# Optimization experiments

Measured on AMD Instinct MI355X. Metric: run time of the kernel, lower is better.

Reference implementation:

```python
import jax, jax.numpy as jnp
import numpy as np

N_NODES = 1024
CHANNELS = [1, 64, 128]
DENSE = [196608, 256]
SAMPLE_NUMBER = 50


def _glorot(key, shape):
    fan_in, fan_out = shape[0], shape[-1]
    s = jnp.sqrt(6.0 / (fan_in + fan_out))
    return jax.random.uniform(key, shape, jnp.float32, -s, s)


def setup_inputs() -> dict:
    key = jax.random.key(0)
    ks = jax.random.split(key, 20)
    T, B = 16, 64
    inp = {
        "xs_seq": jax.random.normal(ks[0], (T, B, N_NODES, CHANNELS[0]), jnp.float32),
        "adj": jax.random.uniform(ks[1], (N_NODES, N_NODES), jnp.float32) / N_NODES,
    }
    # GCGRU params per layer: gates z, r, candidate n over concat([x, h])
    ki = 2
    for li in range(len(CHANNELS) - 1):
        cin, cout = CHANNELS[li], CHANNELS[li + 1]
        for g in ("z", "r", "n"):
            inp[f"W{g}{li}"] = _glorot(ks[ki], (cin + cout, cout)); ki += 1
            inp[f"b{g}{li}"] = jnp.zeros((cout,), jnp.float32)
    inp["W_mu"] = _glorot(ks[ki], (DENSE[0], DENSE[1])); ki += 1
    inp["b_mu"] = jnp.zeros((DENSE[1],), jnp.float32)
    inp["W_lv"] = _glorot(ks[ki], (DENSE[0], DENSE[1])); ki += 1
    inp["b_lv"] = jnp.zeros((DENSE[1],), jnp.float32)
    return inp


def _gcgru(xs, adj, Wz, bz, Wr, br, Wn, bn, cout):
    # xs: [T, B, N, cin]; graph-conv GRU over time via scan
    T, B, N, _ = xs.shape
    h0 = jnp.zeros((B, N, cout), xs.dtype)

    def gconv(a, x, W, b):  # adj @ x @ W + b
        return jnp.einsum("ij,bjc,cd->bid", a, x, W) + b

    def step(h, x):
        xh = jnp.concatenate([x, h], axis=-1)
        z = jax.nn.sigmoid(gconv(adj, xh, Wz, bz))
        r = jax.nn.sigmoid(gconv(adj, xh, Wr, br))
        xrh = jnp.concatenate([x, r * h], axis=-1)
        n = jnp.tanh(gconv(adj, xrh, Wn, bn))
        h_new = (1.0 - z) * h + z * n
        return h_new, h_new

    _, hs = jax.lax.scan(step, h0, xs)
    return hs  # [T, B, N, cout]


def _forward(xs_seq, adj, Wz0, bz0, Wr0, br0, Wn0, bn0,
             Wz1, bz1, Wr1, br1, Wn1, bn1, W_mu, b_mu, W_lv, b_lv, eps):
    h1 = _gcgru(xs_seq, adj, Wz0, bz0, Wr0, br0, Wn0, bn0, CHANNELS[1])
    h2 = _gcgru(h1, adj, Wz1, bz1, Wr1, br1, Wn1, bn1, CHANNELS[2])
    xs = jnp.concatenate([h1[-1], h2[-1]], axis=2)  # [B, N, C1+C2]
    B = xs.shape[0]
    xs = xs.reshape(B, -1)  # [B, N*(C1+C2)]
    mu = jax.nn.sigmoid(xs @ W_mu + b_mu)
    logvar = jax.nn.sigmoid(xs @ W_lv + b_lv)
    std = jnp.exp(0.5 * logvar)
    z = mu + eps * std
    return z, mu, logvar


def reference(xs_seq, adj, Wz0, bz0, Wr0, br0, Wn0, bn0,
              Wz1, bz1, Wr1, br1, Wn1, bn1, W_mu, b_mu, W_lv, b_lv):
    B = xs_seq.shape[1]
    ekey = jax.random.fold_in(jax.random.key(0), 1234)
    eps = jax.random.normal(ekey, (SAMPLE_NUMBER, B, DENSE[1]), jnp.float32).mean(0)
    return _forward(xs_seq, adj, Wz0, bz0, Wr0, br0, Wn0, bn0,
                    Wz1, bz1, Wr1, br1, Wn1, bn1, W_mu, b_mu, W_lv, b_lv, eps)
```

## Files before the change

kernel.cpp:

```cpp
#include <hip/hip_runtime.h>
#include <math.h>

#define EPS_MODE 0

typedef unsigned short u16;
typedef short bf16x8 __attribute__((ext_vector_type(8)));
typedef float f32x4 __attribute__((ext_vector_type(4)));
typedef u16 u16x4 __attribute__((ext_vector_type(4)));
typedef u16 u16x8 __attribute__((ext_vector_type(8)));

static constexpr int T = 16;
static constexpr size_t MF = 1u << 20;
static constexpr int DKCH = 256;
static constexpr int DKCHUNK = 196608 / DKCH;

__device__ __forceinline__ u16 f2bf(float f) {
  unsigned u = __float_as_uint(f);
  unsigned r = (u + 0x7fffu + ((u >> 16) & 1u)) >> 16;
  return (u16)r;
}
__device__ __forceinline__ float bf2f(u16 h) {
  return __uint_as_float(((unsigned)h) << 16);
}
__device__ __forceinline__ void gload16(const void* g, void* l) {
  __builtin_amdgcn_global_load_lds(
      (const __attribute__((address_space(1))) void*)g,
      (__attribute__((address_space(3))) void*)l, 16, 0, 0);
}

__global__ __launch_bounds__(256) void cast_bf16(const float* __restrict__ in,
                                                 u16* __restrict__ out, int n) {
  int i = (blockIdx.x * 256 + threadIdx.x) * 4;
  if (i < n) {
    float4 v = *reinterpret_cast<const float4*>(&in[i]);
    out[i + 0] = f2bf(v.x); out[i + 1] = f2bf(v.y);
    out[i + 2] = f2bf(v.z); out[i + 3] = f2bf(v.w);
  }
}

__global__ __launch_bounds__(256) void prep_wt(const float* __restrict__ Wz0, const float* __restrict__ Wr0,
                                               const float* __restrict__ Wn0, const float* __restrict__ Wz1,
                                               const float* __restrict__ Wr1, const float* __restrict__ Wn1,
                                               u16* __restrict__ WzrT0, u16* __restrict__ WnT0,
                                               u16* __restrict__ WzrT1, u16* __restrict__ WnT1) {
  int seg = blockIdx.y;
  int idx = blockIdx.x * 256 + threadIdx.x;
  if (seg == 0) {
    if (idx < 128 * 64) {
      int j = idx >> 6, k = idx & 63;
      float v = (j < 64) ? Wz0[(k + 1) * 64 + j] : Wr0[(k + 1) * 64 + (j - 64)];
      WzrT0[idx] = f2bf(v);
    }
  } else if (seg == 1) {
    if (idx < 64 * 64) {
      int j = idx >> 6, k = idx & 63;
      WnT0[idx] = f2bf(Wn0[(k + 1) * 64 + j]);
    }
  } else if (seg == 2) {
    if (idx < 256 * 192) {
      int j = idx / 192, k = idx % 192;
      float v = (j < 128) ? Wz1[k * 128 + j] : Wr1[k * 128 + (j - 128)];
      WzrT1[idx] = f2bf(v);
    }
  } else {
    if (idx < 128 * 192) {
      int j = idx / 192, k = idx % 192;
      WnT1[idx] = f2bf(Wn1[k * 128 + j]);
    }
  }
}

template <int EPI, int LOGC, int MFR>
__global__ __launch_bounds__(256) void adj_mfma(const u16* __restrict__ A,
                                                const u16* __restrict__ BT,
                                                void* __restrict__ OUT) {
  constexpr int MT = MFR * 32;
  __shared__ __align__(16) char lds[(MFR + 4) * 4096];
  int tid = threadIdx.x;
  int w = tid >> 6, lane = tid & 63;
  int row0 = blockIdx.y * MT, col0 = blockIdx.x * 128;
  int wm = w >> 1, wn = w & 1;
  f32x4 acc[MFR][4] = {};
  for (int k0 = 0; k0 < 1024; k0 += 64) {
#pragma unroll
    for (int q = 0; q < MFR; ++q) {
      int row = q * 32 + w * 8 + (lane >> 3);
      gload16(A + (size_t)(row0 + row) * 1024 + k0 + (lane & 7) * 8,
              lds + q * 4096 + w * 1024);
    }
#pragma unroll
    for (int q = 0; q < 4; ++q) {
      int row = q * 32 + w * 8 + (lane >> 3);
      gload16(BT + (size_t)(col0 + row) * 1024 + k0 + (lane & 7) * 8,
              lds + MFR * 4096 + q * 4096 + w * 1024);
    }
    __syncthreads();
#pragma unroll
    for (int kk = 0; kk < 2; ++kk) {
      bf16x8 a[MFR], bb[4];
#pragma unroll
      for (int m = 0; m < MFR; ++m)
        a[m] = *(const bf16x8*)(lds + (wm * (MFR * 16) + m * 16 + (lane & 15)) * 128 + kk * 64 + (lane >> 4) * 16);
#pragma unroll
      for (int n = 0; n < 4; ++n)
        bb[n] = *(const bf16x8*)(lds + MFR * 4096 + (wn * 64 + n * 16 + (lane & 15)) * 128 + kk * 64 + (lane >> 4) * 16);
#pragma unroll
      for (int m = 0; m < MFR; ++m)
#pragma unroll
        for (int n = 0; n < 4; ++n)
          acc[m][n] = __builtin_amdgcn_mfma_f32_16x16x32_bf16(a[m], bb[n], acc[m][n], 0, 0, 0);
    }
    __syncthreads();
  }
  if (EPI == 1) {
    float* O = (float*)OUT;
#pragma unroll
    for (int m = 0; m < MFR; ++m)
#pragma unroll
      for (int n = 0; n < 4; ++n) {
        int col = col0 + wn * 64 + n * 16 + (lane & 15);
        int t = col >> 6, bbx = col & 63;
        int row = row0 + wm * (MFR * 16) + m * 16 + ((lane >> 4) << 2);
        *(float4*)&O[((size_t)t << 16) + ((size_t)bbx << 10) + row] = *(float4*)&acc[m][n];
      }
  } else {
    u16* O = (u16*)OUT;
    constexpr int C = 1 << LOGC;
#pragma unroll
    for (int m = 0; m < MFR; ++m)
#pragma unroll
      for (int n = 0; n < 4; ++n) {
        int col = col0 + wn * 64 + n * 16 + (lane & 15);
        int bbx = col >> LOGC, c = col & (C - 1);
#pragma unroll
        for (int j = 0; j < 4; ++j) {
          int row = row0 + wm * (MFR * 16) + m * 16 + ((lane >> 4) << 2) + j;
          O[(((size_t)bbx << 10) + row) * C + c] = f2bf(acc[m][n][j]);
        }
      }
  }
}

template <int C, int RK1, int MFR>
__global__ __launch_bounds__(256) void adj_ngate(
    const u16* __restrict__ A, const u16* __restrict__ BT,
    const u16* __restrict__ WnT, const float* __restrict__ bias,
    const float* __restrict__ axv, const float* __restrict__ wx,
    const u16* __restrict__ AH1, const u16* __restrict__ zT,
    u16* __restrict__ hT) {
  constexpr int LOGC = (C == 64) ? 6 : 7;
  constexpr int KW = (C == 64) ? 64 : 192;
  constexpr int KKAN = C / 32;
  constexpr int MT = MFR * 32;
  constexpr int STG = (MFR + 4) * 4096;
  constexpr int ANBYTES = MT * 136 * 2;
  constexpr int LDSZ = STG > ANBYTES ? STG : ANBYTES;
  __shared__ __align__(16) char lds[LDSZ];
  int tid = threadIdx.x;
  int w = tid >> 6, lane = tid & 63;
  int row0 = blockIdx.y * MT, col0 = blockIdx.x * 128;
  int wm = w >> 1, wn = w & 1;
  f32x4 acc[MFR][4] = {};
  for (int k0 = 0; k0 < 1024; k0 += 64) {
#pragma unroll
    for (int q = 0; q < MFR; ++q) {
      int row = q * 32 + w * 8 + (lane >> 3);
      gload16(A + (size_t)(row0 + row) * 1024 + k0 + (lane & 7) * 8,
              lds + q * 4096 + w * 1024);
    }
#pragma unroll
    for (int q = 0; q < 4; ++q) {
      int row = q * 32 + w * 8 + (lane >> 3);
      gload16(BT + (size_t)(col0 + row) * 1024 + k0 + (lane & 7) * 8,
              lds + MFR * 4096 + q * 4096 + w * 1024);
    }
    __syncthreads();
#pragma unroll
    for (int kk = 0; kk < 2; ++kk) {
      bf16x8 a[MFR], bb[4];
#pragma unroll
      for (int m = 0; m < MFR; ++m)
        a[m] = *(const bf16x8*)(lds + (wm * (MFR * 16) + m * 16 + (lane & 15)) * 128 + kk * 64 + (lane >> 4) * 16);
#pragma unroll
      for (int n = 0; n < 4; ++n)
        bb[n] = *(const bf16x8*)(lds + MFR * 4096 + (wn * 64 + n * 16 + (lane & 15)) * 128 + kk * 64 + (lane >> 4) * 16);
#pragma unroll
      for (int m = 0; m < MFR; ++m)
#pragma unroll
        for (int n = 0; n < 4; ++n)
          acc[m][n] = __builtin_amdgcn_mfma_f32_16x16x32_bf16(a[m], bb[n], acc[m][n], 0, 0, 0);
    }
    __syncthreads();
  }
  u16* ANt = (u16*)lds;
#pragma unroll
  for (int m = 0; m < MFR; ++m)
#pragma unroll
    for (int n = 0; n < 4; ++n) {
      int cl = wn * 64 + n * 16 + (lane & 15);
      int rl = wm * (MFR * 16) + m * 16 + ((lane >> 4) << 2);
#pragma unroll
      for (int j = 0; j < 4; ++j)
        ANt[(rl + j) * 136 + cl] = f2bf(acc[m][n][j]);
    }
  __syncthreads();
  int wrow = w >> 1, half = w & 1;
  int arow0 = wrow * (MFR * 16);
  int b0 = col0 >> LOGC;
  int out0 = (C == 64) ? 0 : half * 64;
  int kbase = (C == 64) ? half * 64 : 0;
  int b_eff = (C == 64) ? (b0 + half) : b0;
  constexpr int WOFF = (C == 64) ? 0 : 64;
  f32x4 acc2[MFR][4] = {};
#pragma unroll
  for (int kk = 0; kk < KKAN; ++kk) {
    bf16x8 a[MFR], bb[4];
    int ka = kbase + kk * 32 + (lane >> 4) * 8;
#pragma unroll
    for (int m = 0; m < MFR; ++m)
      a[m] = *(const bf16x8*)&ANt[(arow0 + m * 16 + (lane & 15)) * 136 + ka];
#pragma unroll
    for (int n = 0; n < 4; ++n)
      bb[n] = *(const bf16x8*)&WnT[(size_t)(out0 + n * 16 + (lane & 15)) * KW + WOFF + kk * 32 + (lane >> 4) * 8];
#pragma unroll
    for (int m = 0; m < MFR; ++m)
#pragma unroll
      for (int n = 0; n < 4; ++n)
        acc2[m][n] = __builtin_amdgcn_mfma_f32_16x16x32_bf16(a[m], bb[n], acc2[m][n], 0, 0, 0);
  }
  if (C == 128) {
#pragma unroll
    for (int kk = 0; kk < 2; ++kk) {
      bf16x8 a[MFR], bb[4];
#pragma unroll
      for (int m = 0; m < MFR; ++m)
        a[m] = *(const bf16x8*)&AH1[(((size_t)b0 << 10) + row0 + arow0 + m * 16 + (lane & 15)) * 64 + kk * 32 + (lane >> 4) * 8];
#pragma unroll
      for (int n = 0; n < 4; ++n)
        bb[n] = *(const bf16x8*)&WnT[(size_t)(out0 + n * 16 + (lane & 15)) * 192 + kk * 32 + (lane >> 4) * 8];
#pragma unroll
      for (int m = 0; m < MFR; ++m)
#pragma unroll
        for (int n = 0; n < 4; ++n)
          acc2[m][n] = __builtin_amdgcn_mfma_f32_16x16x32_bf16(a[m], bb[n], acc2[m][n], 0, 0, 0);
    }
  }
#pragma unroll
  for (int m = 0; m < MFR; ++m) {
    float ax4[4];
    if (RK1) {
      float4 v = *(const float4*)&axv[((size_t)b_eff << 10) + row0 + arow0 + m * 16 + ((lane >> 4) << 2)];
      ax4[0] = v.x; ax4[1] = v.y; ax4[2] = v.z; ax4[3] = v.w;
    }
#pragma unroll
    for (int n = 0; n < 4; ++n) {
      int cp = out0 + n * 16 + (lane & 15);
      int grow = arow0 + m * 16 + ((lane >> 4) << 2);
      size_t idx = (((size_t)b_eff << LOGC) + cp) * 1024 + row0 + grow;
      u16x4 zv = *(const u16x4*)&zT[idx];
      u16x4 hv = *(const u16x4*)&hT[idx];
      u16x4 pk;
#pragma unroll
      for (int j = 0; j < 4; ++j) {
        float g = acc2[m][n][j] + bias[cp];
        if (RK1) g += ax4[j] * wx[cp];
        float nv = tanhf(g);
        float z = bf2f(zv[j]), ho = bf2f(hv[j]);
        pk[j] = f2bf((1.f - z) * ho + z * nv);
      }
      *(u16x4*)&hT[idx] = pk;
    }
  }
}

template <int WM, int WN, int C, int NK1, int NK, int RK1>
__global__ __launch_bounds__(256) void gate_zr(
    const u16* __restrict__ A1, const u16* __restrict__ A2,
    const u16* __restrict__ WT, const float* __restrict__ bz,
    const float* __restrict__ br, const float* __restrict__ axv,
    const float* __restrict__ wxz, const float* __restrict__ wxr,
    const u16* __restrict__ hT, u16* __restrict__ zTo, u16* __restrict__ rhTo) {
  constexpr int MT = WM * 64, NT = WN * 64, K = NK * 64;
  constexpr int NB = 1024 / MT;
  __shared__ __align__(16) char lds[MT * 128 + NT * 128];
  int tid = threadIdx.x;
  int w = tid >> 6, lane = tid & 63;
  int by = blockIdx.x;
  int b = by / NB, n0 = (by % NB) * MT;
  size_t row0 = ((size_t)b << 10) + n0;
  int wm = w / WN, wn = w % WN;
  f32x4 acc[4][4] = {};
  for (int s = 0; s < NK; ++s) {
    const u16* As; int astr, koff;
    if (s < NK1) { As = A1; astr = 64; koff = s * 64; }
    else         { As = A2; astr = 128; koff = (s - NK1) * 64; }
#pragma unroll
    for (int q = 0; q < MT / 32; ++q) {
      int row = q * 32 + w * 8 + (lane >> 3);
      gload16(As + (row0 + row) * astr + koff + (lane & 7) * 8,
              lds + q * 4096 + w * 1024);
    }
#pragma unroll
    for (int q = 0; q < NT / 32; ++q) {
      int row = q * 32 + w * 8 + (lane >> 3);
      gload16(WT + (size_t)row * K + s * 64 + (lane & 7) * 8,
              lds + MT * 128 + q * 4096 + w * 1024);
    }
    __syncthreads();
#pragma unroll
    for (int kk = 0; kk < 2; ++kk) {
      bf16x8 a[4], bb[4];
#pragma unroll
      for (int m = 0; m < 4; ++m)
        a[m] = *(const bf16x8*)(lds + (wm * 64 + m * 16 + (lane & 15)) * 128 + kk * 64 + (lane >> 4) * 16);
#pragma unroll
      for (int n = 0; n < 4; ++n)
        bb[n] = *(const bf16x8*)(lds + MT * 128 + (wn * 64 + n * 16 + (lane & 15)) * 128 + kk * 64 + (lane >> 4) * 16);
#pragma unroll
      for (int m = 0; m < 4; ++m)
#pragma unroll
        for (int n = 0; n < 4; ++n)
          acc[m][n] = __builtin_amdgcn_mfma_f32_16x16x32_bf16(a[m], bb[n], acc[m][n], 0, 0, 0);
    }
    __syncthreads();
  }
#pragma unroll
  for (int m = 0; m < 4; ++m) {
    float ax4[4];
    if (RK1) {
      float4 v = *(const float4*)&axv[row0 + wm * 64 + m * 16 + ((lane >> 4) << 2)];
      ax4[0] = v.x; ax4[1] = v.y; ax4[2] = v.z; ax4[3] = v.w;
    }
#pragma unroll
    for (int n = 0; n < 4; ++n) {
      int cp = wn * 64 + n * 16 + (lane & 15);
      bool iz = cp < C;
      int c = iz ? cp : cp - C;
      int rl = wm * 64 + m * 16 + ((lane >> 4) << 2);
      size_t idx = (((size_t)b * C + c) << 10) + n0 + rl;
      u16x4 hv;
      if (!iz) hv = *(const u16x4*)&hT[idx];
      u16x4 pk;
#pragma unroll
      for (int j = 0; j < 4; ++j) {
        float g = acc[m][n][j] + (iz ? bz : br)[c];
        if (RK1) g += ax4[j] * (iz ? wxz : wxr)[c];
        float sg = 1.f / (1.f + expf(-g));
        pk[j] = iz ? f2bf(sg) : f2bf(sg * bf2f(hv[j]));
      }
      *(u16x4*)&(iz ? zTo : rhTo)[idx] = pk;
    }
  }
}

__global__ __launch_bounds__(256) void transpose_x(const u16* __restrict__ h1T,
                                                   const u16* __restrict__ h2T,
                                                   u16* __restrict__ X) {
  int b = blockIdx.x;
  int n0 = blockIdx.y * 128;
  __shared__ u16 tile[192][136];
  int tid = threadIdx.x;
#pragma unroll
  for (int i = 0; i < 12; ++i) {
    int id = tid + i * 256;
    int c = id >> 4, g = id & 15;
    u16x8 v;
    if (c < 64) v = *(const u16x8*)&h1T[(((size_t)b << 6) + c) * 1024 + n0 + g * 8];
    else        v = *(const u16x8*)&h2T[(((size_t)b << 7) + (c - 64)) * 1024 + n0 + g * 8];
    *(u16x8*)&tile[c][g * 8] = v;
  }
  __syncthreads();
#pragma unroll
  for (int i = 0; i < 12; ++i) {
    int id = tid + i * 256;
    int n = id / 24, g = id % 24;
    u16x8 v;
#pragma unroll
    for (int j = 0; j < 8; ++j) v[j] = tile[g * 8 + j][n];
    *(u16x8*)&X[(size_t)b * 196608 + (size_t)(n0 + n) * 192 + g * 8] = v;
  }
}

__global__ __launch_bounds__(256) void dense_mfma2(const u16* __restrict__ X,
                                                   const float* __restrict__ Wmu,
                                                   const float* __restrict__ Wlv,
                                                   float* __restrict__ P) {
  __shared__ __align__(16) char lds[8192 + 256 * 70 * 2];
  u16* Bs = (u16*)(lds + 8192);
  int tid = threadIdx.x, w = tid >> 6, lane = tid & 63;
  int ch = blockIdx.x, mat = blockIdx.y;
  const float* W = mat ? Wlv : Wmu;
  int kb = ch * DKCHUNK;
  int oL = tid & 63;
  f32x4 acc[4][4] = {};
  for (int s = 0; s < DKCHUNK / 64; ++s) {
    int kg = kb + s * 64;
#pragma unroll
    for (int q = 0; q < 2; ++q) {
      int row = q * 32 + w * 8 + (lane >> 3);
      gload16(X + (size_t)row * 196608 + kg + (lane & 7) * 8,
              lds + q * 4096 + w * 1024);
    }
#pragma unroll
    for (int og = 0; og < 4; ++og) {
      int o = og * 64 + oL;
      float v[16];
#pragma unroll
      for (int kk = 0; kk < 16; ++kk)
        v[kk] = W[(size_t)(kg + w * 16 + kk) * 256 + o];
      u16x8 p0, p1;
#pragma unroll
      for (int j = 0; j < 8; ++j) p0[j] = f2bf(v[j]);
#pragma unroll
      for (int j = 0; j < 8; ++j) p1[j] = f2bf(v[8 + j]);
      *(u16x8*)&Bs[o * 70 + w * 16] = p0;
      *(u16x8*)&Bs[o * 70 + w * 16 + 8] = p1;
    }
    __syncthreads();
#pragma unroll
    for (int kk = 0; kk < 2; ++kk) {
      bf16x8 a[4], bb[4];
#pragma unroll
      for (int m = 0; m < 4; ++m)
        a[m] = *(const bf16x8*)(lds + (m * 16 + (lane & 15)) * 128 + kk * 64 + (lane >> 4) * 16);
#pragma unroll
      for (int n = 0; n < 4; ++n) {
        int o = w * 64 + n * 16 + (lane & 15);
        bb[n] = *(const bf16x8*)&Bs[o * 70 + kk * 32 + (lane >> 4) * 8];
      }
#pragma unroll
      for (int m = 0; m < 4; ++m)
#pragma unroll
        for (int n = 0; n < 4; ++n)
          acc[m][n] = __builtin_amdgcn_mfma_f32_16x16x32_bf16(a[m], bb[n], acc[m][n], 0, 0, 0);
    }
    __syncthreads();
  }
#pragma unroll
  for (int m = 0; m < 4; ++m)
#pragma unroll
    for (int n = 0; n < 4; ++n) {
      int o = w * 64 + n * 16 + (lane & 15);
#pragma unroll
      for (int j = 0; j < 4; ++j) {
        int row = m * 16 + ((lane >> 4) << 2) + j;
        P[(((size_t)mat * DKCH + ch) * 64 + row) * 256 + o] = acc[m][n][j];
      }
    }
}

__device__ __forceinline__ unsigned rotl32(unsigned v, int s) {
  return (v << s) | (v >> (32 - s));
}
__device__ void threefry(unsigned k0, unsigned k1, unsigned x0, unsigned x1,
                         unsigned& o0, unsigned& o1) {
  unsigned ks2 = k0 ^ k1 ^ 0x1BD11BDAu;
  unsigned a = x0 + k0, b = x1 + k1;
#define TF_RND(rot) { a += b; b = rotl32(b, rot); b ^= a; }
  TF_RND(13) TF_RND(15) TF_RND(26) TF_RND(6)
  a += k1; b += ks2 + 1u;
  TF_RND(17) TF_RND(29) TF_RND(16) TF_RND(24)
  a += ks2; b += k0 + 2u;
  TF_RND(13) TF_RND(15) TF_RND(26) TF_RND(6)
  a += k0; b += k1 + 3u;
  TF_RND(17) TF_RND(29) TF_RND(16) TF_RND(24)
  a += k1; b += ks2 + 4u;
  TF_RND(13) TF_RND(15) TF_RND(26) TF_RND(6)
  a += ks2; b += k0 + 5u;
#undef TF_RND
  o0 = a; o1 = b;
}

__device__ float u32_to_normal(unsigned bits) {
  unsigned fb = (bits >> 9) | 0x3F800000u;
  float f = __uint_as_float(fb) - 1.0f;
  const float lo = -0.99999994f;
  float u = f * 2.0f + lo;
  u = fmaxf(lo, u);
  float w = -log1pf(-u * u);
  float p;
  if (w < 5.0f) {
    w -= 2.5f;
    p = 2.81022636e-08f;
    p = fmaf(p, w, 3.43273939e-07f);
    p = fmaf(p, w, -3.5233877e-06f);
    p = fmaf(p, w, -4.39150654e-06f);
    p = fmaf(p, w, 0.00021858087f);
    p = fmaf(p, w, -0.00125372503f);
    p = fmaf(p, w, -0.00417768164f);
    p = fmaf(p, w, 0.246640727f);
    p = fmaf(p, w, 1.50140941f);
  } else {
    w = sqrtf(w) - 3.0f;
    p = -0.000200214257f;
    p = fmaf(p, w, 0.000100950558f);
    p = fmaf(p, w, 0.00134934322f);
    p = fmaf(p, w, -0.00367342844f);
    p = fmaf(p, w, 0.00573950773f);
    p = fmaf(p, w, -0.0076224613f);
    p = fmaf(p, w, 0.00943887047f);
    p = fmaf(p, w, 1.00167406f);
    p = fmaf(p, w, 2.83297682f);
  }
  return 1.41421354f * (p * u);
}

__global__ __launch_bounds__(256) void eps_kernel(float* __restrict__ eps) {
  int b = blockIdx.x;
  int o = threadIdx.x;
  unsigned k0, k1;
  threefry(0u, 0u, 0u, 1234u, k0, k1);
  float s = 0.f;
  for (int smp = 0; smp < 50; ++smp) {
    unsigned idx = ((unsigned)smp * 64u + (unsigned)b) * 256u + (unsigned)o;
    unsigned o0, o1, bits;
#if EPS_MODE == 0
    threefry(k0, k1, 0u, idx, o0, o1);
    bits = o0 ^ o1;
#else
    unsigned pp = idx % 409600u, half = idx / 409600u;
    threefry(k0, k1, pp, pp + 409600u, o0, o1);
    bits = half ? o1 : o0;
#endif
    s += u32_to_normal(bits);
  }
  eps[b * 256 + o] = s / 50.0f;
}

__global__ __launch_bounds__(256) void final_kernel(const float* __restrict__ P,
                                                    const float* __restrict__ bmu,
                                                    const float* __restrict__ blv,
                                                    const float* __restrict__ eps,
                                                    float* __restrict__ out) {
  int b = blockIdx.x, o = threadIdx.x;
  float smu = 0.f, slv = 0.f;
  for (int ch = 0; ch < DKCH; ++ch) {
    smu += P[(((size_t)0 * DKCH + ch) * 64 + b) * 256 + o];
    slv += P[(((size_t)1 * DKCH + ch) * 64 + b) * 256 + o];
  }
  float mu = 1.f / (1.f + expf(-(smu + bmu[o])));
  float lv = 1.f / (1.f + expf(-(slv + blv[o])));
  float z = mu + eps[b * 256 + o] * expf(0.5f * lv);
  out[b * 256 + o] = z;
  out[16384 + b * 256 + o] = mu;
  out[32768 + b * 256 + o] = lv;
}

extern "C" void kernel_launch(void* const* d_in, const int* in_sizes, int n_in,
                              void* d_out, int out_size, void* d_ws, size_t ws_size,
                              hipStream_t stream) {
  (void)in_sizes; (void)n_in; (void)out_size; (void)ws_size;
  const float* xs  = (const float*)d_in[0];
  const float* adj = (const float*)d_in[1];
  const float* Wz0 = (const float*)d_in[2];  const float* bz0 = (const float*)d_in[3];
  const float* Wr0 = (const float*)d_in[4];  const float* br0 = (const float*)d_in[5];
  const float* Wn0 = (const float*)d_in[6];  const float* bn0 = (const float*)d_in[7];
  const float* Wz1 = (const float*)d_in[8];  const float* bz1 = (const float*)d_in[9];
  const float* Wr1 = (const float*)d_in[10]; const float* br1 = (const float*)d_in[11];
  const float* Wn1 = (const float*)d_in[12]; const float* bn1 = (const float*)d_in[13];
  const float* Wmu = (const float*)d_in[14]; const float* bmu = (const float*)d_in[15];
  const float* Wlv = (const float*)d_in[16]; const float* blv = (const float*)d_in[17];

  float* ws = (float*)d_ws;
  u16*  adjB  = (u16*)(ws);
  u16*  xsB   = (u16*)(ws + MF / 2);
  float* AXv  = ws + 1 * MF;
  u16*  h1T   = (u16*)(ws + 2 * MF);
  u16*  h2T   = (u16*)(ws + 4 * MF);
  u16*  z0T   = (u16*)(ws + 8 * MF);
  u16*  z1T   = (u16*)(ws + 10 * MF);
  u16*  rh0T  = (u16*)(ws + 14 * MF);
  u16*  rh1T  = (u16*)(ws + 16 * MF);
  u16*  AH1   = (u16*)(ws + 20 * MF);
  u16*  AH2   = (u16*)(ws + 22 * MF);
  u16*  WTb   = (u16*)(ws + 26 * MF);
  u16*  X     = (u16*)(ws + 8 * MF);
  float* P    = ws + 16 * MF;
  float* EPS  = ws + 24 * MF;

  u16* WzrT0 = WTb;
  u16* WnT0  = WTb + 8192;
  u16* WzrT1 = WTb + 12288;
  u16* WnT1  = WTb + 61440;

  hipMemsetAsync(ws + 2 * MF, 0, 6 * MF * sizeof(float), stream);
  hipMemsetAsync(ws + 20 * MF, 0, 6 * MF * sizeof(float), stream);

  cast_bf16<<<1024, 256, 0, stream>>>(adj, adjB, 1 << 20);
  cast_bf16<<<1024, 256, 0, stream>>>(xs, xsB, 1 << 20);
  prep_wt<<<dim3(192, 4), 256, 0, stream>>>(Wz0, Wr0, Wn0, Wz1, Wr1, Wn1,
                                            WzrT0, WnT0, WzrT1, WnT1);

  adj_mfma<1, 0, 4><<<dim3(8, 8), 256, 0, stream>>>(adjB, xsB, AXv);

  for (int t = 0; t < T; ++t) {
    const float* AXt = AXv + (size_t)t * 65536;
    gate_zr<2, 2, 64, 1, 1, 1><<<512, 256, 0, stream>>>(
        AH1, nullptr, WzrT0, bz0, br0, AXt, Wz0, Wr0, h1T, z0T, rh0T);
    adj_ngate<64, 1, 2><<<dim3(32, 16), 256, 0, stream>>>(
        adjB, rh0T, WnT0, bn0, AXt, Wn0, nullptr, z0T, h1T);
    adj_mfma<0, 6, 2><<<dim3(32, 16), 256, 0, stream>>>(adjB, h1T, AH1);
    gate_zr<1, 4, 128, 1, 3, 0><<<1024, 256, 0, stream>>>(
        AH1, AH2, WzrT1, bz1, br1, nullptr, nullptr, nullptr, h2T, z1T, rh1T);
    adj_ngate<128, 0, 4><<<dim3(64, 8), 256, 0, stream>>>(
        adjB, rh1T, WnT1, bn1, nullptr, nullptr, AH1, z1T, h2T);
    if (t + 1 < T)
      adj_mfma<0, 7, 4><<<dim3(64, 8), 256, 0, stream>>>(adjB, h2T, AH2);
  }

  transpose_x<<<dim3(64, 8), 256, 0, stream>>>(h1T, h2T, X);
  dense_mfma2<<<dim3(DKCH, 2), 256, 0, stream>>>(X, Wmu, Wlv, P);
  eps_kernel<<<64, 256, 0, stream>>>(EPS);
  final_kernel<<<64, 256, 0, stream>>>(P, bmu, blv, EPS, (float*)d_out);
}
```

Before: 2.919 ms.

## Fuse adj@h1 with layer-1 and next-step layer-0 z/r gates; split dense output

Adds a fused kernel that computes adj@h1 via MFMA, stages the result in LDS, and immediately applies the layer-1 z/r gate GEMM plus the next timestep's layer-0 z/r gates. This removes two separate gate_zr launches per timestep and their global round-trips of AH1. The first layer-0 gate is hoisted before the loop. The dense kernel is also split across two output halves, doubling grid size to raise occupancy at the cost of re-reading X. The fused kernel does more work per block and uses more registers, which may lower occupancy.

```diff
diff --git a/kernel.cpp b/kernel.cpp
--- a/kernel.cpp
+++ b/kernel.cpp
@@ -27,6 +27,7 @@
       (const __attribute__((address_space(1))) void*)g,
       (__attribute__((address_space(3))) void*)l, 16, 0, 0);
 }
+__device__ __forceinline__ float sigm(float x) { return 1.f / (1.f + expf(-x)); }
 
 __global__ __launch_bounds__(256) void cast_bf16(const float* __restrict__ in,
                                                  u16* __restrict__ out, int n) {
@@ -345,10 +346,177 @@
       for (int j = 0; j < 4; ++j) {
         float g = acc[m][n][j] + (iz ? bz : br)[c];
         if (RK1) g += ax4[j] * (iz ? wxz : wxr)[c];
-        float sg = 1.f / (1.f + expf(-g));
+        float sg = sigm(g);
         pk[j] = iz ? f2bf(sg) : f2bf(sg * bf2f(hv[j]));
       }
       *(u16x4*)&(iz ? zTo : rhTo)[idx] = pk;
+    }
+  }
+}
+
+__global__ __launch_bounds__(256) void ah1_zr(
+    const u16* __restrict__ adjB, const u16* __restrict__ h1T,
+    const u16* __restrict__ AH2, const u16* __restrict__ h2T,
+    const u16* __restrict__ WzrT1, const float* __restrict__ bz1, const float* __restrict__ br1,
+    const u16* __restrict__ WzrT0, const float* __restrict__ bz0, const float* __restrict__ br0,
+    const float* __restrict__ AXt1, const float* __restrict__ wz0x, const float* __restrict__ wr0x,
+    u16* __restrict__ AH1, u16* __restrict__ z1T, u16* __restrict__ rh1T,
+    u16* __restrict__ z0T, u16* __restrict__ rh0T, int do_zr0) {
+  __shared__ __align__(16) char lds[24576];
+  int tid = threadIdx.x, w = tid >> 6, lane = tid & 63;
+  int row0 = blockIdx.y * 64, col0 = blockIdx.x * 128;
+  int b0 = col0 >> 6;
+  int wm = w >> 1, wn = w & 1;
+  f32x4 acc[2][4] = {};
+  for (int k0 = 0; k0 < 1024; k0 += 64) {
+#pragma unroll
+    for (int q = 0; q < 2; ++q) {
+      int row = q * 32 + w * 8 + (lane >> 3);
+      gload16(adjB + (size_t)(row0 + row) * 1024 + k0 + (lane & 7) * 8,
+              lds + q * 4096 + w * 1024);
+    }
+#pragma unroll
+    for (int q = 0; q < 4; ++q) {
+      int row = q * 32 + w * 8 + (lane >> 3);
+      gload16(h1T + (size_t)(col0 + row) * 1024 + k0 + (lane & 7) * 8,
+              lds + 8192 + q * 4096 + w * 1024);
+    }
+    __syncthreads();
+#pragma unroll
+    for (int kk = 0; kk < 2; ++kk) {
+      bf16x8 a[2], bb[4];
+#pragma unroll
+      for (int m = 0; m < 2; ++m)
+        a[m] = *(const bf16x8*)(lds + (wm * 32 + m * 16 + (lane & 15)) * 128 + kk * 64 + (lane >> 4) * 16);
+#pragma unroll
+      for (int n = 0; n < 4; ++n)
+        bb[n] = *(const bf16x8*)(lds + 8192 + (wn * 64 + n * 16 + (lane & 15)) * 128 + kk * 64 + (lane >> 4) * 16);
+#pragma unroll
+      for (int m = 0; m < 2; ++m)
+#pragma unroll
+        for (int n = 0; n < 4; ++n)
+          acc[m][n] = __builtin_amdgcn_mfma_f32_16x16x32_bf16(a[m], bb[n], acc[m][n], 0, 0, 0);
+    }
+    __syncthreads();
+  }
+  u16* ANt = (u16*)lds;
+#pragma unroll
+  for (int m = 0; m < 2; ++m)
+#pragma unroll
+    for (int n = 0; n < 4; ++n) {
+      int col = wn * 64 + n * 16 + (lane & 15);
+      int bl = col >> 6, c = col & 63;
+      int rl = wm * 32 + m * 16 + ((lane >> 4) << 2);
+#pragma unroll
+      for (int j = 0; j < 4; ++j) {
+        u16 v = f2bf(acc[m][n][j]);
+        AH1[(((size_t)(b0 + bl) << 10) + row0 + rl + j) * 64 + c] = v;
+        ANt[(bl * 64 + rl + j) * 72 + c] = v;
+      }
+    }
+  __syncthreads();
+  int b = b0 + wm;
+#pragma unroll
+  for (int hz = 0; hz < 2; ++hz) {
+    f32x4 g1[4][4] = {};
+#pragma unroll
+    for (int kk = 0; kk < 2; ++kk) {
+      bf16x8 a[4], bb[4];
+#pragma unroll
+      for (int m = 0; m < 4; ++m)
+        a[m] = *(const bf16x8*)&ANt[(wm * 64 + m * 16 + (lane & 15)) * 72 + kk * 32 + (lane >> 4) * 8];
+#pragma unroll
+      for (int n = 0; n < 4; ++n) {
+        int out = hz * 128 + wn * 64 + n * 16 + (lane & 15);
+        bb[n] = *(const bf16x8*)&WzrT1[(size_t)out * 192 + kk * 32 + (lane >> 4) * 8];
+      }
+#pragma unroll
+      for (int m = 0; m < 4; ++m)
+#pragma unroll
+        for (int n = 0; n < 4; ++n)
+          g1[m][n] = __builtin_amdgcn_mfma_f32_16x16x32_bf16(a[m], bb[n], g1[m][n], 0, 0, 0);
+    }
+#pragma unroll
+    for (int kk = 0; kk < 4; ++kk) {
+      bf16x8 a[4], bb[4];
+#pragma unroll
+      for (int m = 0; m < 4; ++m) {
+        int gn = row0 + m * 16 + (lane & 15);
+        a[m] = *(const bf16x8*)&AH2[(((size_t)b << 10) + gn) * 128 + kk * 32 + (lane >> 4) * 8];
+      }
+#pragma unroll
+      for (int n = 0; n < 4; ++n) {
+        int out = hz * 128 + wn * 64 + n * 16 + (lane & 15);
+        bb[n] = *(const bf16x8*)&WzrT1[(size_t)out * 192 + 64 + kk * 32 + (lane >> 4) * 8];
+      }
+#pragma unroll
+      for (int m = 0; m < 4; ++m)
+#pragma unroll
+        for (int n = 0; n < 4; ++n)
+          g1[m][n] = __builtin_amdgcn_mfma_f32_16x16x32_bf16(a[m], bb[n], g1[m][n], 0, 0, 0);
+    }
+#pragma unroll
+    for (int m = 0; m < 4; ++m)
+#pragma unroll
+      for (int n = 0; n < 4; ++n) {
+        int outq = hz * 128 + wn * 64 + n * 16 + (lane & 15);
+        bool iz = outq < 128;
+        int c = iz ? outq : outq - 128;
+        int gr = m * 16 + ((lane >> 4) << 2);
+        size_t idx = (((size_t)b * 128 + c) << 10) + row0 + gr;
+        u16x4 hv;
+        if (!iz) hv = *(const u16x4*)&h2T[idx];
+        u16x4 pk;
+#pragma unroll
+        for (int j = 0; j < 4; ++j) {
+          float g = g1[m][n][j] + (iz ? bz1 : br1)[c];
+          float sg = sigm(g);
+          pk[j] = iz ? f2bf(sg) : f2bf(sg * bf2f(hv[j]));
+        }
+        *(u16x4*)&(iz ? z1T : rh1T)[idx] = pk;
+      }
+  }
+  if (do_zr0) {
+    f32x4 g0[4][4] = {};
+#pragma unroll
+    for (int kk = 0; kk < 2; ++kk) {
+      bf16x8 a[4], bb[4];
+#pragma unroll
+      for (int m = 0; m < 4; ++m)
+        a[m] = *(const bf16x8*)&ANt[(wm * 64 + m * 16 + (lane & 15)) * 72 + kk * 32 + (lane >> 4) * 8];
+#pragma unroll
+      for (int n = 0; n < 4; ++n) {
+        int out = wn * 64 + n * 16 + (lane & 15);
+        bb[n] = *(const bf16x8*)&WzrT0[(size_t)out * 64 + kk * 32 + (lane >> 4) * 8];
+      }
+#pragma unroll
+      for (int m = 0; m < 4; ++m)
+#pragma unroll
+        for (int n = 0; n < 4; ++n)
+          g0[m][n] = __builtin_amdgcn_mfma_f32_16x16x32_bf16(a[m], bb[n], g0[m][n], 0, 0, 0);
+    }
+#pragma unroll
+    for (int m = 0; m < 4; ++m) {
+      int gr0 = m * 16 + ((lane >> 4) << 2);
+      float4 av = *(const float4*)&AXt1[((size_t)b << 10) + row0 + gr0];
+      float ax4[4] = {av.x, av.y, av.z, av.w};
+#pragma unroll
+      for (int n = 0; n < 4; ++n) {
+        int out = wn * 64 + n * 16 + (lane & 15);
+        bool iz = out < 64;
+        int c = out & 63;
+        size_t idx = (((size_t)b * 64 + c) << 10) + row0 + gr0;
+        u16x4 hv;
+        if (!iz) hv = *(const u16x4*)&h1T[idx];
+        u16x4 pk;
+#pragma unroll
+        for (int j = 0; j < 4; ++j) {
+          float g = g0[m][n][j] + (iz ? bz0 : br0)[c] + ax4[j] * (iz ? wz0x : wr0x)[c];
+          float sg = sigm(g);
+          pk[j] = iz ? f2bf(sg) : f2bf(sg * bf2f(hv[j]));
+        }
+        *(u16x4*)&(iz ? z0T : rh0T)[idx] = pk;
+      }
     }
   }
 }
@@ -381,18 +549,19 @@
   }
 }
 
-__global__ __launch_bounds__(256) void dense_mfma2(const u16* __restrict__ X,
+__global__ __launch_bounds__(256) void dense_mfma3(const u16* __restrict__ X,
                                                    const float* __restrict__ Wmu,
                                                    const float* __restrict__ Wlv,
                                                    float* __restrict__ P) {
-  __shared__ __align__(16) char lds[8192 + 256 * 70 * 2];
+  __shared__ __align__(16) char lds[8192 + 128 * 70 * 2];
   u16* Bs = (u16*)(lds + 8192);
   int tid = threadIdx.x, w = tid >> 6, lane = tid & 63;
-  int ch = blockIdx.x, mat = blockIdx.y;
+  int o0 = blockIdx.x * 128;
+  int ch = blockIdx.y, mat = blockIdx.z;
   const float* W = mat ? Wlv : Wmu;
   int kb = ch * DKCHUNK;
   int oL = tid & 63;
-  f32x4 acc[4][4] = {};
+  f32x4 acc[4][2] = {};
   for (int s = 0; s < DKCHUNK / 64; ++s) {
     int kg = kb + s * 64;
 #pragma unroll
@@ -402,12 +571,12 @@
               lds + q * 4096 + w * 1024);
     }
 #pragma unroll
-    for (int og = 0; og < 4; ++og) {
+    for (int og = 0; og < 2; ++og) {
       int o = og * 64 + oL;
       float v[16];
 #pragma unroll
       for (int kk = 0; kk < 16; ++kk)
-        v[kk] = W[(size_t)(kg + w * 16 + kk) * 256 + o];
+        v[kk] = W[(size_t)(kg + w * 16 + kk) * 256 + o0 + o];
       u16x8 p0, p1;
 #pragma unroll
       for (int j = 0; j < 8; ++j) p0[j] = f2bf(v[j]);
@@ -419,19 +588,19 @@
     __syncthreads();
 #pragma unroll
     for (int kk = 0; kk < 2; ++kk) {
-      bf16x8 a[4], bb[4];
+      bf16x8 a[4], bb[2];
 #pragma unroll
       for (int m = 0; m < 4; ++m)
         a[m] = *(const bf16x8*)(lds + (m * 16 + (lane & 15)) * 128 + kk * 64 + (lane >> 4) * 16);
 #pragma unroll
-      for (int n = 0; n < 4; ++n) {
-        int o = w * 64 + n * 16 + (lane & 15);
+      for (int n = 0; n < 2; ++n) {
+        int o = w * 32 + n * 16 + (lane & 15);
         bb[n] = *(const bf16x8*)&Bs[o * 70 + kk * 32 + (lane >> 4) * 8];
       }
 #pragma unroll
       for (int m = 0; m < 4; ++m)
 #pragma unroll
-        for (int n = 0; n < 4; ++n)
+        for (int n = 0; n < 2; ++n)
           acc[m][n] = __builtin_amdgcn_mfma_f32_16x16x32_bf16(a[m], bb[n], acc[m][n], 0, 0, 0);
     }
     __syncthreads();
@@ -439,8 +608,8 @@
 #pragma unroll
   for (int m = 0; m < 4; ++m)
 #pragma unroll
-    for (int n = 0; n < 4; ++n) {
-      int o = w * 64 + n * 16 + (lane & 15);
+    for (int n = 0; n < 2; ++n) {
+      int o = o0 + w * 32 + n * 16 + (lane & 15);
 #pragma unroll
       for (int j = 0; j < 4; ++j) {
         int row = m * 16 + ((lane >> 4) << 2) + j;
@@ -538,8 +707,8 @@
     smu += P[(((size_t)0 * DKCH + ch) * 64 + b) * 256 + o];
     slv += P[(((size_t)1 * DKCH + ch) * 64 + b) * 256 + o];
   }
-  float mu = 1.f / (1.f + expf(-(smu + bmu[o])));
-  float lv = 1.f / (1.f + expf(-(slv + blv[o])));
+  float mu = sigm(smu + bmu[o]);
+  float lv = sigm(slv + blv[o]);
   float z = mu + eps[b * 256 + o] * expf(0.5f * lv);
   out[b * 256 + o] = z;
   out[16384 + b * 256 + o] = mu;
@@ -593,15 +762,17 @@
 
   adj_mfma<1, 0, 4><<<dim3(8, 8), 256, 0, stream>>>(adjB, xsB, AXv);
 
+  gate_zr<2, 2, 64, 1, 1, 1><<<512, 256, 0, stream>>>(
+      AH1, nullptr, WzrT0, bz0, br0, AXv, Wz0, Wr0, h1T, z0T, rh0T);
+
   for (int t = 0; t < T; ++t) {
     const float* AXt = AXv + (size_t)t * 65536;
-    gate_zr<2, 2, 64, 1, 1, 1><<<512, 256, 0, stream>>>(
-        AH1, nullptr, WzrT0, bz0, br0, AXt, Wz0, Wr0, h1T, z0T, rh0T);
+    const float* AXn = AXv + (size_t)((t + 1 < T) ? t + 1 : t) * 65536;
     adj_ngate<64, 1, 2><<<dim3(32, 16), 256, 0, stream>>>(
         adjB, rh0T, WnT0, bn0, AXt, Wn0, nullptr, z0T, h1T);
-    adj_mfma<0, 6, 2><<<dim3(32, 16), 256, 0, stream>>>(adjB, h1T, AH1);
-    gate_zr<1, 4, 128, 1, 3, 0><<<1024, 256, 0, stream>>>(
-        AH1, AH2, WzrT1, bz1, br1, nullptr, nullptr, nullptr, h2T, z1T, rh1T);
+    ah1_zr<<<dim3(32, 16), 256, 0, stream>>>(
+        adjB, h1T, AH2, h2T, WzrT1, bz1, br1, WzrT0, bz0, br0,
+        AXn, Wz0, Wr0, AH1, z1T, rh1T, z0T, rh0T, (t + 1 < T) ? 1 : 0);
     adj_ngate<128, 0, 4><<<dim3(64, 8), 256, 0, stream>>>(
         adjB, rh1T, WnT1, bn1, nullptr, nullptr, AH1, z1T, h2T);
     if (t + 1 < T)
@@ -609,7 +780,7 @@
   }
 
   transpose_x<<<dim3(64, 8), 256, 0, stream>>>(h1T, h2T, X);
-  dense_mfma2<<<dim3(DKCH, 2), 256, 0, stream>>>(X, Wmu, Wlv, P);
+  dense_mfma3<<<dim3(2, DKCH, 2), 256, 0, stream>>>(X, Wmu, Wlv, P);
   eps_kernel<<<64, 256, 0, stream>>>(EPS);
   final_kernel<<<64, 256, 0, stream>>>(P, bmu, blv, EPS, (float*)d_out);
 }
```

Measured after the change: 2.784 ms. -4.6%, faster.
